# Optimization experiments

Hardware: AMD Instinct MI355X
Metric: run time of the kernel (lower is better)

The kernel has to match this reference:

```python
import jax, jax.numpy as jnp
import numpy as np

N = 8192  # nv + nh, bias=False


def setup_inputs() -> dict:
    key = jax.random.key(0)
    k1, k2, k3, k4 = jax.random.split(key, 4)
    w = jax.random.normal(k1, (N, N), dtype=jnp.float32) * 0.01  # learned [n,n] coupling matrix
    initial_state = jax.random.randint(k2, (N,), 0, 2).astype(jnp.float32)  # binary unit states
    clamping_degree = jnp.zeros((N,), dtype=jnp.float32)  # 0 => unit is free to update
    T = jnp.float32(1.0)  # temperature
    perm = jax.random.permutation(k3, N).astype(jnp.int32)  # torch.randperm(self.n)
    rand_u = jax.random.uniform(k4, (N,), dtype=jnp.float32)  # torch.rand(1) per unit
    return {"w": w, "initial_state": initial_state, "clamping_degree": clamping_degree,
            "T": T, "perm": perm, "rand_u": rand_u}


def reference(w, initial_state, clamping_degree, T, perm, rand_u):
    # Sequential Gibbs sweep: for each j in perm, if unclamped,
    # p = sigmoid(w[j]@state / T); state[j] = 1 if u <= p else 0.
    inactive = jnp.float32(0.0)

    def step(state, ju):
        j, u = ju
        sum_input = jnp.dot(w[j], state)          # per-unit dot product against current state
        p = jax.nn.sigmoid(sum_input / T)          # 1/(1+exp(-x/T))
        new_val = jnp.where(u <= p, jnp.float32(1.0), inactive)
        upd = jnp.where(clamping_degree[j] == 0, new_val, state[j])
        return state.at[j].set(upd), None

    final_state, _ = jax.lax.scan(step, initial_state, (perm, rand_u))
    return final_state
```

## Files before the change

kernel.cpp:

```cpp
#include <hip/hip_runtime.h>
#include <math.h>


#define NN 8192
#define BB 512
#define NBLK 16
#define SUB 64
#define NSUB 8
#define NWG 256
#define NWORK 255
#define TPB 512
#define MAXR 3

typedef unsigned int u32;

__global__ void k_init(u32* flags, int n) {
  int i = blockIdx.x * blockDim.x + threadIdx.x;
  for (; i < n; i += gridDim.x * blockDim.x) flags[i] = 0;
}

__device__ __forceinline__ u32 ld_rlx(const u32* p) {
  return __hip_atomic_load(p, __ATOMIC_RELAXED, __HIP_MEMORY_SCOPE_AGENT);
}
__device__ __forceinline__ void st_rlx(u32* p, u32 v) {
  __hip_atomic_store(p, v, __ATOMIC_RELAXED, __HIP_MEMORY_SCOPE_AGENT);
}
__device__ __forceinline__ float ldf_rlx(const float* p) {
  return __hip_atomic_load(p, __ATOMIC_RELAXED, __HIP_MEMORY_SCOPE_AGENT);
}
__device__ __forceinline__ void stf_rlx(float* p, float v) {
  __hip_atomic_store(p, v, __ATOMIC_RELAXED, __HIP_MEMORY_SCOPE_AGENT);
}
__device__ __forceinline__ double ldd_rlx(const double* p) {
  return __hip_atomic_load(p, __ATOMIC_RELAXED, __HIP_MEMORY_SCOPE_AGENT);
}
__device__ __forceinline__ void std_rlx(double* p, double v) {
  __hip_atomic_store(p, v, __ATOMIC_RELAXED, __HIP_MEMORY_SCOPE_AGENT);
}

#define LOADM(MARR, T8N) do {                                                  \
  const float4* mr_ = (const float4*)(tb + (size_t)((T8N) * SUB + tid) * BB + (T8N) * SUB); \
  _Pragma("unroll")                                                            \
  for (int j_ = 0; j_ < SUB / 4; ++j_) {                                       \
    float4 v_ = mr_[j_];                                                       \
    MARR[4*j_] = v_.x; MARR[4*j_+1] = v_.y;                                    \
    MARR[4*j_+2] = v_.z; MARR[4*j_+3] = v_.w; }                                \
} while (0)

#define CHAIN(MARR, T8C) do {                                                  \
  int row_ = (T8C) * SUB + tid;                                                \
  double sum_ = sumsL[row_], th_ = thrL[row_];                                 \
  float dd1_ = d1L[row_], dd0_ = d0L[row_];                                    \
  float mydel_ = 0.0f;                                                         \
  __builtin_amdgcn_s_setprio(3);                                               \
  _Pragma("unroll")                                                            \
  for (int s_ = 0; s_ < SUB; ++s_) {                                           \
    float down_ = (sum_ >= th_) ? dd1_ : dd0_;                                 \
    float sd_ = __uint_as_float(                                               \
        __builtin_amdgcn_readlane(__float_as_uint(down_), s_));                \
    if (s_ == tid) mydel_ = down_;                                             \
    sum_ += (double)(MARR[s_] * sd_); }                                        \
  __builtin_amdgcn_s_setprio(0);                                               \
  delL[row_] = mydel_;                                                         \
  if (pub) stf_rlx(&delG[b * BB + row_], mydel_);                              \
} while (0)

__global__ __launch_bounds__(TPB) void k_gibbs(
    const float* __restrict__ w, const float* __restrict__ init,
    const float* __restrict__ clampv, const float* __restrict__ Tp,
    const int* __restrict__ perm, const float* __restrict__ urand,
    float* __restrict__ dout, double* __restrict__ S,
    float* __restrict__ delG, float* __restrict__ tileD,
    u32* subFlag, u32* ack) {
  __shared__ float stateL[NN];
  __shared__ double sumsL[BB], thrL[BB];
  __shared__ float d1L[BB], d0L[BB], delL[BB], oldL[BB];
  __shared__ int uL[BB];
  __shared__ double redL[TPB / 64][MAXR];
  const int wg = blockIdx.x, tid = threadIdx.x;
  const int wv = tid >> 6, lane = tid & 63;

  if (wg == 0) {
    double T = (double)Tp[0];
    for (int b = 0; b < NBLK; ++b) {
      const bool pub = (b + 1 < NBLK);
      int pos = b * BB + tid;
      int unit = perm[pos];
      double uu = (double)urand[pos];
      thrL[tid] = T * log(uu / (1.0 - uu));
      float old = init[unit];
      bool cl = (clampv[unit] != 0.0f);
      d1L[tid] = cl ? 0.0f : (1.0f - old);
      d0L[tid] = cl ? 0.0f : (0.0f - old);
      oldL[tid] = old;
      uL[tid] = unit;
      {
        const u32* slots = ack + (size_t)b * NWORK;
        for (;;) {
          int ok = 1;
          if (tid < NWORK) ok = (ld_rlx(&slots[tid]) != 0u);
          if (__syncthreads_and(ok)) break;
          __builtin_amdgcn_s_sleep(1);
        }
      }
      sumsL[tid] = ldd_rlx(&S[(size_t)b * BB + tid]);
      __syncthreads();
      const float* tb = tileD + (size_t)b * BB * BB;
      float mA[SUB], mB[SUB];
      float4 nv0, nv1, nv2, nv3;
      if (tid < SUB) LOADM(mA, 0);

      for (int t8 = 0; t8 < NSUB; ++t8) {
        if (t8 > 0) {
          if (pub && tid == 0) st_rlx(&subFlag[b * NSUB + (t8 - 1)], 1u);
          if (tid >= 256) {
            int t = tid - 256;
            int rrow = t8 * SUB + (t >> 2);
            int q = t & 3;
            int c0 = (t8 - 1) * SUB + q * 16;
            double p_ =
                (double)(nv0.x * delL[c0])    + (double)(nv0.y * delL[c0+1]) +
                (double)(nv0.z * delL[c0+2])  + (double)(nv0.w * delL[c0+3]) +
                (double)(nv1.x * delL[c0+4])  + (double)(nv1.y * delL[c0+5]) +
                (double)(nv1.z * delL[c0+6])  + (double)(nv1.w * delL[c0+7]);
            p_ +=
                (double)(nv2.x * delL[c0+8])  + (double)(nv2.y * delL[c0+9]) +
                (double)(nv2.z * delL[c0+10]) + (double)(nv2.w * delL[c0+11]) +
                (double)(nv3.x * delL[c0+12]) + (double)(nv3.y * delL[c0+13]) +
                (double)(nv3.z * delL[c0+14]) + (double)(nv3.w * delL[c0+15]);
            p_ += __shfl_down(p_, 2, 4);
            p_ += __shfl_down(p_, 1, 4);
            if (q == 0) sumsL[rrow] += p_;
          }
        }
        __syncthreads();
        if (tid < SUB) {
          if (t8 & 1) { if (t8 < NSUB - 1) LOADM(mA, t8 + 1); CHAIN(mB, t8); }
          else        { if (t8 < NSUB - 1) LOADM(mB, t8 + 1); CHAIN(mA, t8); }
        } else {
          if (t8 < NSUB - 1 && tid >= 256) {
            int t = tid - 256;
            const float4* pr = (const float4*)(
                tb + (size_t)((t8 + 1) * SUB + (t >> 2)) * BB + t8 * SUB + (t & 3) * 16);
            nv0 = pr[0]; nv1 = pr[1]; nv2 = pr[2]; nv3 = pr[3];
          }
          if (t8 > 0) {
            for (int r = (t8 + 1) * SUB + (tid - SUB); r < BB; r += (TPB - SUB)) {
              int c0 = (t8 - 1) * SUB;
              const float4* mr3 = (const float4*)(tb + (size_t)r * BB + c0);
              double acc = sumsL[r];
#pragma unroll
              for (int j = 0; j < SUB / 4; ++j) {
                float4 v = mr3[j];
                acc += (double)(v.x * delL[c0+4*j])   + (double)(v.y * delL[c0+4*j+1]) +
                       (double)(v.z * delL[c0+4*j+2]) + (double)(v.w * delL[c0+4*j+3]);
              }
              sumsL[r] = acc;
            }
          }
        }
        __syncthreads();
      }
      if (pub && tid == 0) st_rlx(&subFlag[b * NSUB + (NSUB - 1)], 1u);
      dout[uL[tid]] = oldL[tid] + delL[tid];
    }
  } else {
    const int iw = wg - 1;
    const int r0 = (iw * BB) / NWORK, r1 = ((iw + 1) * BB) / NWORK;
    const int cnt = r1 - r0;
    for (int i = tid; i < NN; i += TPB) stateL[i] = init[i];
    __syncthreads();

    for (int p = 0; p < NBLK; ++p) {
      int pc = perm[p * BB + tid];
      float g[NSUB];
      float* tbp = tileD + (size_t)p * BB * BB;

      for (int ri = 0; ri < cnt; ++ri) {
        int unit = perm[p * BB + r0 + ri];
        const float* wrow = w + (size_t)unit * NN;
        const float4* wr4 = (const float4*)wrow;
        const float4* st4 = (const float4*)stateL;
        double acc = 0.0;
#pragma unroll
        for (int k = 0; k < NN / (4 * TPB); ++k) {
          float4 a = wr4[tid + k * TPB];
          float4 s = st4[tid + k * TPB];
          acc += (double)(a.x * s.x) + (double)(a.y * s.y) +
                 (double)(a.z * s.z) + (double)(a.w * s.w);
        }
        for (int o = 32; o > 0; o >>= 1) acc += __shfl_down(acc, o, 64);
        if (lane == 0) redL[wv][ri] = acc;
        stf_rlx(&tbp[(size_t)(r0 + ri) * BB + tid], wrow[pc]);
        if (p > 0 && wv == ri) {
#pragma unroll
          for (int t8 = 0; t8 < NSUB; ++t8)
            g[t8] = wrow[perm[(p - 1) * BB + t8 * SUB + lane]];
        }
      }
      __syncthreads();
      double Sr = 0.0;
      if (wv < cnt) {
#pragma unroll
        for (int k = 0; k < TPB / 64; ++k) Sr += redL[k][wv];
      }
      if (p > 0) {
        double crr = 0.0;
        for (int t8 = 0; t8 < NSUB; ++t8) {
          const u32* f = &subFlag[(p - 1) * NSUB + t8];
          if (tid == 0) {
            while (ld_rlx(f) == 0u) __builtin_amdgcn_s_sleep(1);
          }
          __syncthreads();
          float dl = ldf_rlx(&delG[(p - 1) * BB + t8 * SUB + lane]);
          if (wv < cnt) crr += (double)(g[t8] * dl);
          if (tid < SUB) stateL[perm[(p - 1) * BB + t8 * SUB + tid]] += dl;
        }
        for (int o = 32; o > 0; o >>= 1) crr += __shfl_down(crr, o, 64);
        Sr += crr;
      }
      if (wv < cnt && lane == 0) std_rlx(&S[(size_t)p * BB + r0 + wv], Sr);
      __syncthreads();
      if (tid == 0) st_rlx(&ack[(size_t)p * NWORK + iw], 1u);
    }
  }
}

extern "C" void kernel_launch(void* const* d_in, const int* in_sizes, int n_in,
                              void* d_out, int out_size, void* d_ws, size_t ws_size,
                              hipStream_t stream) {
  const float* w      = (const float*)d_in[0];
  const float* init   = (const float*)d_in[1];
  const float* clampv = (const float*)d_in[2];
  const float* Tp     = (const float*)d_in[3];
  const int*   perm   = (const int*)d_in[4];
  const float* urand  = (const float*)d_in[5];
  float* dout = (float*)d_out;

  double* S    = (double*)d_ws;
  float* delG  = (float*)(S + NN);
  float* tileD = delG + NN;
  u32* subFlag = (u32*)(tileD + (size_t)NBLK * BB * BB);
  u32* ack     = subFlag + NBLK * NSUB;

  int nflags = NBLK * NSUB + NBLK * NWORK;
  k_init<<<8, 256, 0, stream>>>(subFlag, nflags);

  void* args[] = {(void*)&w, (void*)&init, (void*)&clampv, (void*)&Tp,
                  (void*)&perm, (void*)&urand, (void*)&dout,
                  (void*)&S, (void*)&delG, (void*)&tileD,
                  (void*)&subFlag, (void*)&ack};
  hipLaunchCooperativeKernel((const void*)k_gibbs, dim3(NWG), dim3(TPB),
                             args, 0, stream);
}
```

Baseline: 508.6 us.

## Decouple worker blocks from last sub-block and stage diagonal tiles in LDS

```diff
diff --git a/kernel.cpp b/kernel.cpp
--- a/kernel.cpp
+++ b/kernel.cpp
@@ -11,8 +11,11 @@
 #define NWORK 255
 #define TPB 512
 #define MAXR 3
+#define MSTR 68
+#define MBUFW (SUB * MSTR)
 
 typedef unsigned int u32;
+typedef unsigned long long u64;
 
 __global__ void k_init(u32* flags, int n) {
   int i = blockIdx.x * blockDim.x + threadIdx.x;
@@ -37,115 +40,143 @@
 __device__ __forceinline__ void std_rlx(double* p, double v) {
   __hip_atomic_store(p, v, __ATOMIC_RELAXED, __HIP_MEMORY_SCOPE_AGENT);
 }
-
-#define LOADM(MARR, T8N) do {                                                  \
-  const float4* mr_ = (const float4*)(tb + (size_t)((T8N) * SUB + tid) * BB + (T8N) * SUB); \
-  _Pragma("unroll")                                                            \
-  for (int j_ = 0; j_ < SUB / 4; ++j_) {                                       \
-    float4 v_ = mr_[j_];                                                       \
-    MARR[4*j_] = v_.x; MARR[4*j_+1] = v_.y;                                    \
-    MARR[4*j_+2] = v_.z; MARR[4*j_+3] = v_.w; }                                \
-} while (0)
-
-#define CHAIN(MARR, T8C) do {                                                  \
-  int row_ = (T8C) * SUB + tid;                                                \
-  double sum_ = sumsL[row_], th_ = thrL[row_];                                 \
-  float dd1_ = d1L[row_], dd0_ = d0L[row_];                                    \
-  float mydel_ = 0.0f;                                                         \
-  __builtin_amdgcn_s_setprio(3);                                               \
-  _Pragma("unroll")                                                            \
-  for (int s_ = 0; s_ < SUB; ++s_) {                                           \
-    float down_ = (sum_ >= th_) ? dd1_ : dd0_;                                 \
-    float sd_ = __uint_as_float(                                               \
-        __builtin_amdgcn_readlane(__float_as_uint(down_), s_));                \
-    if (s_ == tid) mydel_ = down_;                                             \
-    sum_ += (double)(MARR[s_] * sd_); }                                        \
-  __builtin_amdgcn_s_setprio(0);                                               \
-  delL[row_] = mydel_;                                                         \
-  if (pub) stf_rlx(&delG[b * BB + row_], mydel_);                              \
-} while (0)
+__device__ __forceinline__ u64 ldq_rlx(const u64* p) {
+  return __hip_atomic_load(p, __ATOMIC_RELAXED, __HIP_MEMORY_SCOPE_AGENT);
+}
 
 __global__ __launch_bounds__(TPB) void k_gibbs(
     const float* __restrict__ w, const float* __restrict__ init,
     const float* __restrict__ clampv, const float* __restrict__ Tp,
     const int* __restrict__ perm, const float* __restrict__ urand,
-    float* __restrict__ dout, double* __restrict__ S,
-    float* __restrict__ delG, float* __restrict__ tileD,
+    float* __restrict__ dout,
+    double* __restrict__ thrG, double* __restrict__ S,
+    float* __restrict__ d1G, float* __restrict__ d0G,
+    float* __restrict__ oldG, float* __restrict__ delG,
+    float* __restrict__ stripG, float* __restrict__ tileD,
     u32* subFlag, u32* ack) {
-  __shared__ float stateL[NN];
-  __shared__ double sumsL[BB], thrL[BB];
-  __shared__ float d1L[BB], d0L[BB], delL[BB], oldL[BB];
-  __shared__ int uL[BB];
-  __shared__ double redL[TPB / 64][MAXR];
+  __shared__ double poolD[55296 / 8];
   const int wg = blockIdx.x, tid = threadIdx.x;
   const int wv = tid >> 6, lane = tid & 63;
 
   if (wg == 0) {
+    double* sumsL = poolD;
+    double* thrL  = poolD + BB;
+    float*  d1L   = (float*)(poolD + 2 * BB);
+    float*  d0L   = d1L + BB;
+    float*  delL  = d0L + BB;
+    float*  oldL  = delL + BB;
+    int*    uL    = (int*)(oldL + BB);
+    float*  mbuf  = (float*)(uL + BB);
+
     double T = (double)Tp[0];
+    for (int i = tid; i < NN; i += TPB) {
+      int unit = perm[i];
+      double uu = (double)urand[i];
+      std_rlx(&thrG[i], T * log(uu / (1.0 - uu)));
+      float old = init[unit];
+      bool cl = (clampv[unit] != 0.0f);
+      stf_rlx(&d1G[i], cl ? 0.0f : (1.0f - old));
+      stf_rlx(&d0G[i], cl ? 0.0f : (0.0f - old));
+      stf_rlx(&oldG[i], old);
+    }
+    __syncthreads();
+    {
+      const u32* slots = ack;
+      for (;;) {
+        int ok = 1;
+        if (tid < NWORK) ok = (ld_rlx(&slots[tid]) != 0u);
+        if (__syncthreads_and(ok)) break;
+        __builtin_amdgcn_s_sleep(1);
+      }
+    }
+    sumsL[tid] = ldd_rlx(&S[tid]);
+    thrL[tid] = ldd_rlx(&thrG[tid]);
+    d1L[tid] = ldf_rlx(&d1G[tid]);
+    d0L[tid] = ldf_rlx(&d0G[tid]);
+    oldL[tid] = ldf_rlx(&oldG[tid]);
+    uL[tid] = perm[tid];
+    if (tid >= 448) {
+      int l = tid - 448;
+      const float4* src = (const float4*)(tileD + (size_t)l * BB);
+      float4* dst = (float4*)(mbuf + l * MSTR);
+#pragma unroll
+      for (int j = 0; j < 16; ++j) dst[j] = src[j];
+    }
+    __syncthreads();
+
+    float4 nv0, nv1, nv2, nv3;
     for (int b = 0; b < NBLK; ++b) {
       const bool pub = (b + 1 < NBLK);
-      int pos = b * BB + tid;
-      int unit = perm[pos];
-      double uu = (double)urand[pos];
-      thrL[tid] = T * log(uu / (1.0 - uu));
-      float old = init[unit];
-      bool cl = (clampv[unit] != 0.0f);
-      d1L[tid] = cl ? 0.0f : (1.0f - old);
-      d0L[tid] = cl ? 0.0f : (0.0f - old);
-      oldL[tid] = old;
-      uL[tid] = unit;
-      {
-        const u32* slots = ack + (size_t)b * NWORK;
-        for (;;) {
-          int ok = 1;
-          if (tid < NWORK) ok = (ld_rlx(&slots[tid]) != 0u);
-          if (__syncthreads_and(ok)) break;
-          __builtin_amdgcn_s_sleep(1);
-        }
-      }
-      sumsL[tid] = ldd_rlx(&S[(size_t)b * BB + tid]);
-      __syncthreads();
       const float* tb = tileD + (size_t)b * BB * BB;
-      float mA[SUB], mB[SUB];
-      float4 nv0, nv1, nv2, nv3;
-      if (tid < SUB) LOADM(mA, 0);
 
       for (int t8 = 0; t8 < NSUB; ++t8) {
-        if (t8 > 0) {
-          if (pub && tid == 0) st_rlx(&subFlag[b * NSUB + (t8 - 1)], 1u);
-          if (tid >= 256) {
-            int t = tid - 256;
-            int rrow = t8 * SUB + (t >> 2);
-            int q = t & 3;
-            int c0 = (t8 - 1) * SUB + q * 16;
-            double p_ =
-                (double)(nv0.x * delL[c0])    + (double)(nv0.y * delL[c0+1]) +
-                (double)(nv0.z * delL[c0+2])  + (double)(nv0.w * delL[c0+3]) +
-                (double)(nv1.x * delL[c0+4])  + (double)(nv1.y * delL[c0+5]) +
-                (double)(nv1.z * delL[c0+6])  + (double)(nv1.w * delL[c0+7]);
-            p_ +=
-                (double)(nv2.x * delL[c0+8])  + (double)(nv2.y * delL[c0+9]) +
-                (double)(nv2.z * delL[c0+10]) + (double)(nv2.w * delL[c0+11]) +
-                (double)(nv3.x * delL[c0+12]) + (double)(nv3.y * delL[c0+13]) +
-                (double)(nv3.z * delL[c0+14]) + (double)(nv3.w * delL[c0+15]);
-            p_ += __shfl_down(p_, 2, 4);
-            p_ += __shfl_down(p_, 1, 4);
-            if (q == 0) sumsL[rrow] += p_;
-          }
-        }
-        __syncthreads();
+        int o = t8 * SUB;
+        float m[SUB];
+        if (t8 > 0 && pub && tid == 0) st_rlx(&subFlag[b * NSUB + t8 - 1], 1u);
         if (tid < SUB) {
-          if (t8 & 1) { if (t8 < NSUB - 1) LOADM(mA, t8 + 1); CHAIN(mB, t8); }
-          else        { if (t8 < NSUB - 1) LOADM(mB, t8 + 1); CHAIN(mA, t8); }
+          const float4* mr = (const float4*)(mbuf + (t8 & 1) * MBUFW + tid * MSTR);
+#pragma unroll
+          for (int j = 0; j < 16; ++j) {
+            float4 v = mr[j];
+            m[4*j] = v.x; m[4*j+1] = v.y; m[4*j+2] = v.z; m[4*j+3] = v.w;
+          }
+        } else if (t8 > 0 && tid >= 256) {
+          int t = tid - 256, g_ = t >> 2, q = t & 3;
+          int rrow = o + g_;
+          int c0 = (t8 - 1) * SUB + q * 16;
+          double p_ =
+              (double)(nv0.x * delL[c0])    + (double)(nv0.y * delL[c0+1]) +
+              (double)(nv0.z * delL[c0+2])  + (double)(nv0.w * delL[c0+3]) +
+              (double)(nv1.x * delL[c0+4])  + (double)(nv1.y * delL[c0+5]) +
+              (double)(nv1.z * delL[c0+6])  + (double)(nv1.w * delL[c0+7]);
+          p_ +=
+              (double)(nv2.x * delL[c0+8])  + (double)(nv2.y * delL[c0+9]) +
+              (double)(nv2.z * delL[c0+10]) + (double)(nv2.w * delL[c0+11]) +
+              (double)(nv3.x * delL[c0+12]) + (double)(nv3.y * delL[c0+13]) +
+              (double)(nv3.z * delL[c0+14]) + (double)(nv3.w * delL[c0+15]);
+          p_ += __shfl_down(p_, 2, 4);
+          p_ += __shfl_down(p_, 1, 4);
+          if (q == 0) sumsL[rrow] += p_;
+        }
+        __syncthreads();
+        if (tid < SUB) {
+          int row = o + tid;
+          double g = sumsL[row] - thrL[row];
+          float d1v = d1L[row], d0v = d0L[row];
+          u64 xb = 0ull;
+          __builtin_amdgcn_s_setprio(3);
+#pragma unroll
+          for (int s = 0; s < SUB; ++s) {
+            int hi = __builtin_amdgcn_readlane(
+                (int)(__double_as_longlong(g) >> 32), s);
+            int x = (hi >= 0) ? 1 : 0;
+            int a1 = __builtin_amdgcn_readlane((int)__float_as_uint(d1v), s);
+            int a0 = __builtin_amdgcn_readlane((int)__float_as_uint(d0v), s);
+            float sd = __uint_as_float((u32)(x ? a1 : a0));
+            g += (double)(m[s] * sd);
+            xb |= ((u64)x) << s;
+          }
+          __builtin_amdgcn_s_setprio(0);
+          float mydel = ((xb >> tid) & 1ull) ? d1v : d0v;
+          delL[row] = mydel;
+          if (pub) stf_rlx(&delG[b * BB + row], mydel);
+        } else if (tid < 128) {
+          if (t8 < NSUB - 1) {
+            int l = tid - 64, o2 = (t8 + 1) * SUB;
+            const float4* src = (const float4*)(tb + (size_t)(o2 + l) * BB + o2);
+            float4* dst = (float4*)(mbuf + ((t8 + 1) & 1) * MBUFW + l * MSTR);
+#pragma unroll
+            for (int j = 0; j < 16; ++j) dst[j] = src[j];
+          }
         } else {
           if (t8 < NSUB - 1 && tid >= 256) {
             int t = tid - 256;
             const float4* pr = (const float4*)(
-                tb + (size_t)((t8 + 1) * SUB + (t >> 2)) * BB + t8 * SUB + (t & 3) * 16);
+                tb + (size_t)((t8 + 1) * SUB + (t >> 2)) * BB + o + (t & 3) * 16);
             nv0 = pr[0]; nv1 = pr[1]; nv2 = pr[2]; nv3 = pr[3];
           }
           if (t8 > 0) {
-            for (int r = (t8 + 1) * SUB + (tid - SUB); r < BB; r += (TPB - SUB)) {
+            for (int r = (t8 + 1) * SUB + (tid - 128); r < BB; r += 384) {
               int c0 = (t8 - 1) * SUB;
               const float4* mr3 = (const float4*)(tb + (size_t)r * BB + c0);
               double acc = sumsL[r];
@@ -161,10 +192,53 @@
         }
         __syncthreads();
       }
-      if (pub && tid == 0) st_rlx(&subFlag[b * NSUB + (NSUB - 1)], 1u);
+      if (pub && tid == 0) st_rlx(&subFlag[b * NSUB + NSUB - 1], 1u);
       dout[uL[tid]] = oldL[tid] + delL[tid];
+      if (pub) {
+        {
+          const u32* slots = ack + (size_t)(b + 1) * NWORK;
+          for (;;) {
+            int ok = 1;
+            if (tid < NWORK) ok = (ld_rlx(&slots[tid]) != 0u);
+            if (__syncthreads_and(ok)) break;
+            __builtin_amdgcn_s_sleep(1);
+          }
+        }
+        {
+          double acc = ldd_rlx(&S[(size_t)(b + 1) * BB + tid]);
+          const u64* sp = (const u64*)(stripG + ((size_t)(b + 1) * BB + tid) * SUB);
+#pragma unroll
+          for (int k = 0; k < SUB / 2; ++k) {
+            u64 q = ldq_rlx(&sp[k]);
+            float f0 = __uint_as_float((u32)q);
+            float f1 = __uint_as_float((u32)(q >> 32));
+            acc += (double)(f0 * delL[448 + 2 * k]) +
+                   (double)(f1 * delL[448 + 2 * k + 1]);
+          }
+          sumsL[tid] = acc;
+        }
+        {
+          int pos = (b + 1) * BB + tid;
+          thrL[tid] = ldd_rlx(&thrG[pos]);
+          d1L[tid] = ldf_rlx(&d1G[pos]);
+          d0L[tid] = ldf_rlx(&d0G[pos]);
+          oldL[tid] = ldf_rlx(&oldG[pos]);
+          uL[tid] = perm[pos];
+        }
+        if (tid >= 448) {
+          int l = tid - 448;
+          const float4* src = (const float4*)(
+              tileD + (size_t)(b + 1) * BB * BB + (size_t)l * BB);
+          float4* dst = (float4*)(mbuf + l * MSTR);
+#pragma unroll
+          for (int j = 0; j < 16; ++j) dst[j] = src[j];
+        }
+        __syncthreads();
+      }
     }
   } else {
+    float* stateL = (float*)poolD;
+    double* redW = (double*)((char*)poolD + 32768);
     const int iw = wg - 1;
     const int r0 = (iw * BB) / NWORK, r1 = ((iw + 1) * BB) / NWORK;
     const int cnt = r1 - r0;
@@ -172,8 +246,17 @@
     __syncthreads();
 
     for (int p = 0; p < NBLK; ++p) {
+      if (p >= 2) {
+        const u32* f = &subFlag[(p - 2) * NSUB + NSUB - 1];
+        if (tid == 0) { while (ld_rlx(f) == 0u) __builtin_amdgcn_s_sleep(1); }
+        __syncthreads();
+        if (tid < SUB)
+          stateL[perm[(p - 2) * BB + 7 * SUB + tid]] +=
+              ldf_rlx(&delG[(p - 2) * BB + 7 * SUB + tid]);
+        __syncthreads();
+      }
       int pc = perm[p * BB + tid];
-      float g[NSUB];
+      float g[NSUB - 1];
       float* tbp = tileD + (size_t)p * BB * BB;
 
       for (int ri = 0; ri < cnt; ++ri) {
@@ -190,27 +273,28 @@
                  (double)(a.z * s.z) + (double)(a.w * s.w);
         }
         for (int o = 32; o > 0; o >>= 1) acc += __shfl_down(acc, o, 64);
-        if (lane == 0) redL[wv][ri] = acc;
+        if (lane == 0) redW[wv * MAXR + ri] = acc;
         stf_rlx(&tbp[(size_t)(r0 + ri) * BB + tid], wrow[pc]);
         if (p > 0 && wv == ri) {
 #pragma unroll
-          for (int t8 = 0; t8 < NSUB; ++t8)
+          for (int t8 = 0; t8 < NSUB - 1; ++t8)
             g[t8] = wrow[perm[(p - 1) * BB + t8 * SUB + lane]];
+          stf_rlx(&stripG[((size_t)p * BB + r0 + ri) * SUB + lane],
+                  wrow[perm[(p - 1) * BB + 7 * SUB + lane]]);
         }
       }
       __syncthreads();
       double Sr = 0.0;
       if (wv < cnt) {
 #pragma unroll
-        for (int k = 0; k < TPB / 64; ++k) Sr += redL[k][wv];
+        for (int k = 0; k < TPB / 64; ++k) Sr += redW[k * MAXR + wv];
       }
       if (p > 0) {
         double crr = 0.0;
-        for (int t8 = 0; t8 < NSUB; ++t8) {
+#pragma unroll
+        for (int t8 = 0; t8 < NSUB - 1; ++t8) {
           const u32* f = &subFlag[(p - 1) * NSUB + t8];
-          if (tid == 0) {
-            while (ld_rlx(f) == 0u) __builtin_amdgcn_s_sleep(1);
-          }
+          if (tid == 0) { while (ld_rlx(f) == 0u) __builtin_amdgcn_s_sleep(1); }
           __syncthreads();
           float dl = ldf_rlx(&delG[(p - 1) * BB + t8 * SUB + lane]);
           if (wv < cnt) crr += (double)(g[t8] * dl);
@@ -237,9 +321,14 @@
   const float* urand  = (const float*)d_in[5];
   float* dout = (float*)d_out;
 
-  double* S    = (double*)d_ws;
-  float* delG  = (float*)(S + NN);
-  float* tileD = delG + NN;
+  double* thrG = (double*)d_ws;
+  double* S    = thrG + NN;
+  float* d1G   = (float*)(S + NN);
+  float* d0G   = d1G + NN;
+  float* oldG  = d0G + NN;
+  float* delG  = oldG + NN;
+  float* stripG = delG + NN;
+  float* tileD = stripG + (size_t)NBLK * BB * SUB;
   u32* subFlag = (u32*)(tileD + (size_t)NBLK * BB * BB);
   u32* ack     = subFlag + NBLK * NSUB;
 
@@ -248,7 +337,8 @@
 
   void* args[] = {(void*)&w, (void*)&init, (void*)&clampv, (void*)&Tp,
                   (void*)&perm, (void*)&urand, (void*)&dout,
-                  (void*)&S, (void*)&delG, (void*)&tileD,
+                  (void*)&thrG, (void*)&S, (void*)&d1G, (void*)&d0G,
+                  (void*)&oldG, (void*)&delG, (void*)&stripG, (void*)&tileD,
                   (void*)&subFlag, (void*)&ack};
   hipLaunchCooperativeKernel((const void*)k_gibbs, dim3(NWG), dim3(TPB),
                              args, 0, stream);
```

Result: slower. 711.0 us (+39.8%).

## Restructure Gibbs chain with LDS-staged tiles, ballot-based sign test, and coarser sync

Applied to the files above, without the earlier changes.

```diff
diff --git a/kernel.cpp b/kernel.cpp
--- a/kernel.cpp
+++ b/kernel.cpp
@@ -11,8 +11,11 @@
 #define NWORK 255
 #define TPB 512
 #define MAXR 3
+#define MSTR 68
+#define MBUFW (SUB * MSTR)
 
 typedef unsigned int u32;
+typedef unsigned long long u64;
 
 __global__ void k_init(u32* flags, int n) {
   int i = blockIdx.x * blockDim.x + threadIdx.x;
@@ -37,33 +40,6 @@
 __device__ __forceinline__ void std_rlx(double* p, double v) {
   __hip_atomic_store(p, v, __ATOMIC_RELAXED, __HIP_MEMORY_SCOPE_AGENT);
 }
-
-#define LOADM(MARR, T8N) do {                                                  \
-  const float4* mr_ = (const float4*)(tb + (size_t)((T8N) * SUB + tid) * BB + (T8N) * SUB); \
-  _Pragma("unroll")                                                            \
-  for (int j_ = 0; j_ < SUB / 4; ++j_) {                                       \
-    float4 v_ = mr_[j_];                                                       \
-    MARR[4*j_] = v_.x; MARR[4*j_+1] = v_.y;                                    \
-    MARR[4*j_+2] = v_.z; MARR[4*j_+3] = v_.w; }                                \
-} while (0)
-
-#define CHAIN(MARR, T8C) do {                                                  \
-  int row_ = (T8C) * SUB + tid;                                                \
-  double sum_ = sumsL[row_], th_ = thrL[row_];                                 \
-  float dd1_ = d1L[row_], dd0_ = d0L[row_];                                    \
-  float mydel_ = 0.0f;                                                         \
-  __builtin_amdgcn_s_setprio(3);                                               \
-  _Pragma("unroll")                                                            \
-  for (int s_ = 0; s_ < SUB; ++s_) {                                           \
-    float down_ = (sum_ >= th_) ? dd1_ : dd0_;                                 \
-    float sd_ = __uint_as_float(                                               \
-        __builtin_amdgcn_readlane(__float_as_uint(down_), s_));                \
-    if (s_ == tid) mydel_ = down_;                                             \
-    sum_ += (double)(MARR[s_] * sd_); }                                        \
-  __builtin_amdgcn_s_setprio(0);                                               \
-  delL[row_] = mydel_;                                                         \
-  if (pub) stf_rlx(&delG[b * BB + row_], mydel_);                              \
-} while (0)
 
 __global__ __launch_bounds__(TPB) void k_gibbs(
     const float* __restrict__ w, const float* __restrict__ init,
@@ -71,16 +47,21 @@
     const int* __restrict__ perm, const float* __restrict__ urand,
     float* __restrict__ dout, double* __restrict__ S,
     float* __restrict__ delG, float* __restrict__ tileD,
-    u32* subFlag, u32* ack) {
-  __shared__ float stateL[NN];
-  __shared__ double sumsL[BB], thrL[BB];
-  __shared__ float d1L[BB], d0L[BB], delL[BB], oldL[BB];
-  __shared__ int uL[BB];
-  __shared__ double redL[TPB / 64][MAXR];
+    u32* delReady, u32* ack) {
+  __shared__ double poolD[55296 / 8];
   const int wg = blockIdx.x, tid = threadIdx.x;
   const int wv = tid >> 6, lane = tid & 63;
 
   if (wg == 0) {
+    double* sumsL = poolD;
+    double* thrL  = poolD + BB;
+    float*  d1L   = (float*)(poolD + 2 * BB);
+    float*  d0L   = d1L + BB;
+    float*  delL  = d0L + BB;
+    float*  oldL  = delL + BB;
+    int*    uL    = (int*)(oldL + BB);
+    float*  mbuf  = (float*)(uL + BB);
+
     double T = (double)Tp[0];
     for (int b = 0; b < NBLK; ++b) {
       const bool pub = (b + 1 < NBLK);
@@ -104,48 +85,82 @@
         }
       }
       sumsL[tid] = ldd_rlx(&S[(size_t)b * BB + tid]);
+      if (tid >= 448) {
+        int l = tid - 448;
+        const float4* src = (const float4*)(tileD + (size_t)b * BB * BB + (size_t)l * BB);
+        float4* dst = (float4*)(mbuf + l * MSTR);
+#pragma unroll
+        for (int j = 0; j < 16; ++j) dst[j] = src[j];
+      }
       __syncthreads();
       const float* tb = tileD + (size_t)b * BB * BB;
-      float mA[SUB], mB[SUB];
       float4 nv0, nv1, nv2, nv3;
-      if (tid < SUB) LOADM(mA, 0);
 
       for (int t8 = 0; t8 < NSUB; ++t8) {
-        if (t8 > 0) {
-          if (pub && tid == 0) st_rlx(&subFlag[b * NSUB + (t8 - 1)], 1u);
-          if (tid >= 256) {
-            int t = tid - 256;
-            int rrow = t8 * SUB + (t >> 2);
-            int q = t & 3;
-            int c0 = (t8 - 1) * SUB + q * 16;
-            double p_ =
-                (double)(nv0.x * delL[c0])    + (double)(nv0.y * delL[c0+1]) +
-                (double)(nv0.z * delL[c0+2])  + (double)(nv0.w * delL[c0+3]) +
-                (double)(nv1.x * delL[c0+4])  + (double)(nv1.y * delL[c0+5]) +
-                (double)(nv1.z * delL[c0+6])  + (double)(nv1.w * delL[c0+7]);
-            p_ +=
-                (double)(nv2.x * delL[c0+8])  + (double)(nv2.y * delL[c0+9]) +
-                (double)(nv2.z * delL[c0+10]) + (double)(nv2.w * delL[c0+11]) +
-                (double)(nv3.x * delL[c0+12]) + (double)(nv3.y * delL[c0+13]) +
-                (double)(nv3.z * delL[c0+14]) + (double)(nv3.w * delL[c0+15]);
-            p_ += __shfl_down(p_, 2, 4);
-            p_ += __shfl_down(p_, 1, 4);
-            if (q == 0) sumsL[rrow] += p_;
-          }
-        }
-        __syncthreads();
+        int o = t8 * SUB;
+        float m[SUB];
         if (tid < SUB) {
-          if (t8 & 1) { if (t8 < NSUB - 1) LOADM(mA, t8 + 1); CHAIN(mB, t8); }
-          else        { if (t8 < NSUB - 1) LOADM(mB, t8 + 1); CHAIN(mA, t8); }
+          const float4* mr = (const float4*)(mbuf + (t8 & 1) * MBUFW + tid * MSTR);
+#pragma unroll
+          for (int j = 0; j < 16; ++j) {
+            float4 v = mr[j];
+            m[4*j] = v.x; m[4*j+1] = v.y; m[4*j+2] = v.z; m[4*j+3] = v.w;
+          }
+        } else if (t8 > 0 && tid >= 256) {
+          int t = tid - 256, g_ = t >> 2, q = t & 3;
+          int rrow = o + g_;
+          int c0 = (t8 - 1) * SUB + q * 16;
+          double p_ =
+              (double)(nv0.x * delL[c0])    + (double)(nv0.y * delL[c0+1]) +
+              (double)(nv0.z * delL[c0+2])  + (double)(nv0.w * delL[c0+3]) +
+              (double)(nv1.x * delL[c0+4])  + (double)(nv1.y * delL[c0+5]) +
+              (double)(nv1.z * delL[c0+6])  + (double)(nv1.w * delL[c0+7]);
+          p_ +=
+              (double)(nv2.x * delL[c0+8])  + (double)(nv2.y * delL[c0+9]) +
+              (double)(nv2.z * delL[c0+10]) + (double)(nv2.w * delL[c0+11]) +
+              (double)(nv3.x * delL[c0+12]) + (double)(nv3.y * delL[c0+13]) +
+              (double)(nv3.z * delL[c0+14]) + (double)(nv3.w * delL[c0+15]);
+          p_ += __shfl_down(p_, 2, 4);
+          p_ += __shfl_down(p_, 1, 4);
+          if (q == 0) sumsL[rrow] += p_;
+        }
+        __syncthreads();
+        if (tid < SUB) {
+          float d1v = d1L[o + tid], d0v = d0L[o + tid];
+          u64 P1 = __ballot(d1v != 0.0f);
+          u64 M0 = __ballot(d0v != 0.0f);
+          double g = sumsL[o + tid] - thrL[o + tid];
+          u64 xb = 0ull;
+          __builtin_amdgcn_s_setprio(3);
+#pragma unroll
+          for (int s = 0; s < SUB; ++s) {
+            u32 t1 = ((P1 >> s) & 1ull) ? 0x3f800000u : 0u;
+            u32 t0 = ((M0 >> s) & 1ull) ? 0xbf800000u : 0u;
+            int hi = __builtin_amdgcn_readlane(
+                (int)(__double_as_longlong(g) >> 32), s);
+            float sdf = __uint_as_float((hi >= 0) ? t1 : t0);
+            g += (double)(m[s] * sdf);
+            xb |= ((u64)(hi >= 0 ? 1 : 0)) << s;
+          }
+          __builtin_amdgcn_s_setprio(0);
+          delL[o + tid] = ((xb >> tid) & 1ull) ? d1v : d0v;
+        } else if (tid < 128) {
+          if (t8 < NSUB - 1) {
+            int l = tid - 64, o2 = (t8 + 1) * SUB;
+            const float4* src = (const float4*)(tb + (size_t)(o2 + l) * BB + o2);
+            float4* dst = (float4*)(mbuf + ((t8 + 1) & 1) * MBUFW + l * MSTR);
+#pragma unroll
+            for (int j = 0; j < 16; ++j) dst[j] = src[j];
+          }
         } else {
           if (t8 < NSUB - 1 && tid >= 256) {
             int t = tid - 256;
             const float4* pr = (const float4*)(
-                tb + (size_t)((t8 + 1) * SUB + (t >> 2)) * BB + t8 * SUB + (t & 3) * 16);
+                tb + (size_t)((t8 + 1) * SUB + (t >> 2)) * BB + o + (t & 3) * 16);
             nv0 = pr[0]; nv1 = pr[1]; nv2 = pr[2]; nv3 = pr[3];
           }
           if (t8 > 0) {
-            for (int r = (t8 + 1) * SUB + (tid - SUB); r < BB; r += (TPB - SUB)) {
+            for (int r = (t8 + 1) * SUB + (tid - 128); r < BB; r += 384) {
               int c0 = (t8 - 1) * SUB;
               const float4* mr3 = (const float4*)(tb + (size_t)r * BB + c0);
               double acc = sumsL[r];
@@ -161,10 +176,16 @@
         }
         __syncthreads();
       }
-      if (pub && tid == 0) st_rlx(&subFlag[b * NSUB + (NSUB - 1)], 1u);
+      if (pub) {
+        stf_rlx(&delG[b * BB + tid], delL[tid]);
+        __syncthreads();
+        if (tid == 0) st_rlx(&delReady[b], 1u);
+      }
       dout[uL[tid]] = oldL[tid] + delL[tid];
     }
   } else {
+    float* stateL = (float*)poolD;
+    double* redW = (double*)((char*)poolD + 32768);
     const int iw = wg - 1;
     const int r0 = (iw * BB) / NWORK, r1 = ((iw + 1) * BB) / NWORK;
     const int cnt = r1 - r0;
@@ -190,7 +211,7 @@
                  (double)(a.z * s.z) + (double)(a.w * s.w);
         }
         for (int o = 32; o > 0; o >>= 1) acc += __shfl_down(acc, o, 64);
-        if (lane == 0) redL[wv][ri] = acc;
+        if (lane == 0) redW[wv * MAXR + ri] = acc;
         stf_rlx(&tbp[(size_t)(r0 + ri) * BB + tid], wrow[pc]);
         if (p > 0 && wv == ri) {
 #pragma unroll
@@ -202,26 +223,30 @@
       double Sr = 0.0;
       if (wv < cnt) {
 #pragma unroll
-        for (int k = 0; k < TPB / 64; ++k) Sr += redL[k][wv];
+        for (int k = 0; k < TPB / 64; ++k) Sr += redW[k * MAXR + wv];
       }
       if (p > 0) {
+        if (tid == 0) {
+          while (ld_rlx(&delReady[p - 1]) == 0u) __builtin_amdgcn_s_sleep(1);
+        }
+        __syncthreads();
         double crr = 0.0;
-        for (int t8 = 0; t8 < NSUB; ++t8) {
-          const u32* f = &subFlag[(p - 1) * NSUB + t8];
-          if (tid == 0) {
-            while (ld_rlx(f) == 0u) __builtin_amdgcn_s_sleep(1);
-          }
-          __syncthreads();
-          float dl = ldf_rlx(&delG[(p - 1) * BB + t8 * SUB + lane]);
-          if (wv < cnt) crr += (double)(g[t8] * dl);
-          if (tid < SUB) stateL[perm[(p - 1) * BB + t8 * SUB + tid]] += dl;
-        }
-        for (int o = 32; o > 0; o >>= 1) crr += __shfl_down(crr, o, 64);
-        Sr += crr;
+        if (wv < cnt) {
+#pragma unroll
+          for (int t8 = 0; t8 < NSUB; ++t8)
+            crr += (double)(g[t8] * ldf_rlx(&delG[(p - 1) * BB + t8 * SUB + lane]));
+          for (int o = 32; o > 0; o >>= 1) crr += __shfl_down(crr, o, 64);
+          Sr += crr;
+        }
       }
       if (wv < cnt && lane == 0) std_rlx(&S[(size_t)p * BB + r0 + wv], Sr);
       __syncthreads();
       if (tid == 0) st_rlx(&ack[(size_t)p * NWORK + iw], 1u);
+      if (p > 0) {
+        float dl = ldf_rlx(&delG[(p - 1) * BB + tid]);
+        stateL[perm[(p - 1) * BB + tid]] += dl;
+      }
+      __syncthreads();
     }
   }
 }
@@ -238,18 +263,18 @@
   float* dout = (float*)d_out;
 
   double* S    = (double*)d_ws;
-  float* delG  = (float*)(S + NN);
+  float* delG  = (float*)(S + (size_t)NBLK * BB);
   float* tileD = delG + NN;
-  u32* subFlag = (u32*)(tileD + (size_t)NBLK * BB * BB);
-  u32* ack     = subFlag + NBLK * NSUB;
-
-  int nflags = NBLK * NSUB + NBLK * NWORK;
-  k_init<<<8, 256, 0, stream>>>(subFlag, nflags);
+  u32* delReady = (u32*)(tileD + (size_t)NBLK * BB * BB);
+  u32* ack      = delReady + NBLK;
+
+  int nflags = NBLK + NBLK * NWORK;
+  k_init<<<8, 256, 0, stream>>>(delReady, nflags);
 
   void* args[] = {(void*)&w, (void*)&init, (void*)&clampv, (void*)&Tp,
                   (void*)&perm, (void*)&urand, (void*)&dout,
                   (void*)&S, (void*)&delG, (void*)&tileD,
-                  (void*)&subFlag, (void*)&ack};
+                  (void*)&delReady, (void*)&ack};
   hipLaunchCooperativeKernel((const void*)k_gibbs, dim3(NWG), dim3(TPB),
                              args, 0, stream);
 }
```

Result: slower. 589.4 us (+15.9%).

## Move last sub-block correction to sequential WG to shorten critical path

Applied to the files above, without the earlier changes.

```diff
diff --git a/kernel.cpp b/kernel.cpp
--- a/kernel.cpp
+++ b/kernel.cpp
@@ -13,6 +13,7 @@
 #define MAXR 3
 
 typedef unsigned int u32;
+typedef unsigned long long u64;
 
 __global__ void k_init(u32* flags, int n) {
   int i = blockIdx.x * blockDim.x + threadIdx.x;
@@ -30,9 +31,6 @@
 }
 __device__ __forceinline__ void stf_rlx(float* p, float v) {
   __hip_atomic_store(p, v, __ATOMIC_RELAXED, __HIP_MEMORY_SCOPE_AGENT);
-}
-__device__ __forceinline__ double ldd_rlx(const double* p) {
-  return __hip_atomic_load(p, __ATOMIC_RELAXED, __HIP_MEMORY_SCOPE_AGENT);
 }
 __device__ __forceinline__ void std_rlx(double* p, double v) {
   __hip_atomic_store(p, v, __ATOMIC_RELAXED, __HIP_MEMORY_SCOPE_AGENT);
@@ -70,8 +68,8 @@
     const float* __restrict__ clampv, const float* __restrict__ Tp,
     const int* __restrict__ perm, const float* __restrict__ urand,
     float* __restrict__ dout, double* __restrict__ S,
-    float* __restrict__ delG, float* __restrict__ tileD,
-    u32* subFlag, u32* ack) {
+    float* __restrict__ delG, float* __restrict__ stripG,
+    float* __restrict__ tileD, u32* subFlag, u32* ack) {
   __shared__ float stateL[NN];
   __shared__ double sumsL[BB], thrL[BB];
   __shared__ float d1L[BB], d0L[BB], delL[BB], oldL[BB];
@@ -103,7 +101,21 @@
           __builtin_amdgcn_s_sleep(1);
         }
       }
-      sumsL[tid] = ldd_rlx(&S[(size_t)b * BB + tid]);
+      {
+        double acc = S[(size_t)b * BB + tid];
+        if (b > 0) {
+          const float4* sp = (const float4*)(stripG + ((size_t)b * BB + tid) * SUB);
+#pragma unroll
+          for (int k = 0; k < SUB / 4; ++k) {
+            float4 v = sp[k];
+            acc += (double)(v.x * delL[7 * SUB + 4 * k]) +
+                   (double)(v.y * delL[7 * SUB + 4 * k + 1]) +
+                   (double)(v.z * delL[7 * SUB + 4 * k + 2]) +
+                   (double)(v.w * delL[7 * SUB + 4 * k + 3]);
+          }
+        }
+        sumsL[tid] = acc;
+      }
       __syncthreads();
       const float* tb = tileD + (size_t)b * BB * BB;
       float mA[SUB], mB[SUB];
@@ -172,8 +184,17 @@
     __syncthreads();
 
     for (int p = 0; p < NBLK; ++p) {
+      if (p >= 2) {
+        const u32* f = &subFlag[(p - 2) * NSUB + NSUB - 1];
+        if (tid == 0) { while (ld_rlx(f) == 0u) __builtin_amdgcn_s_sleep(1); }
+        __syncthreads();
+        if (tid < SUB)
+          stateL[perm[(p - 2) * BB + 7 * SUB + tid]] +=
+              ldf_rlx(&delG[(p - 2) * BB + 7 * SUB + tid]);
+        __syncthreads();
+      }
       int pc = perm[p * BB + tid];
-      float g[NSUB];
+      float g[NSUB - 1];
       float* tbp = tileD + (size_t)p * BB * BB;
 
       for (int ri = 0; ri < cnt; ++ri) {
@@ -194,8 +215,10 @@
         stf_rlx(&tbp[(size_t)(r0 + ri) * BB + tid], wrow[pc]);
         if (p > 0 && wv == ri) {
 #pragma unroll
-          for (int t8 = 0; t8 < NSUB; ++t8)
+          for (int t8 = 0; t8 < NSUB - 1; ++t8)
             g[t8] = wrow[perm[(p - 1) * BB + t8 * SUB + lane]];
+          stf_rlx(&stripG[((size_t)p * BB + r0 + ri) * SUB + lane],
+                  wrow[perm[(p - 1) * BB + 7 * SUB + lane]]);
         }
       }
       __syncthreads();
@@ -206,11 +229,10 @@
       }
       if (p > 0) {
         double crr = 0.0;
-        for (int t8 = 0; t8 < NSUB; ++t8) {
+#pragma unroll
+        for (int t8 = 0; t8 < NSUB - 1; ++t8) {
           const u32* f = &subFlag[(p - 1) * NSUB + t8];
-          if (tid == 0) {
-            while (ld_rlx(f) == 0u) __builtin_amdgcn_s_sleep(1);
-          }
+          if (tid == 0) { while (ld_rlx(f) == 0u) __builtin_amdgcn_s_sleep(1); }
           __syncthreads();
           float dl = ldf_rlx(&delG[(p - 1) * BB + t8 * SUB + lane]);
           if (wv < cnt) crr += (double)(g[t8] * dl);
@@ -238,8 +260,9 @@
   float* dout = (float*)d_out;
 
   double* S    = (double*)d_ws;
-  float* delG  = (float*)(S + NN);
-  float* tileD = delG + NN;
+  float* delG  = (float*)(S + (size_t)NBLK * BB);
+  float* stripG = delG + NN;
+  float* tileD = stripG + (size_t)NBLK * BB * SUB;
   u32* subFlag = (u32*)(tileD + (size_t)NBLK * BB * BB);
   u32* ack     = subFlag + NBLK * NSUB;
 
@@ -248,7 +271,7 @@
 
   void* args[] = {(void*)&w, (void*)&init, (void*)&clampv, (void*)&Tp,
                   (void*)&perm, (void*)&urand, (void*)&dout,
-                  (void*)&S, (void*)&delG, (void*)&tileD,
+                  (void*)&S, (void*)&delG, (void*)&stripG, (void*)&tileD,
                   (void*)&subFlag, (void*)&ack};
   hipLaunchCooperativeKernel((const void*)k_gibbs, dim3(NWG), dim3(TPB),
                              args, 0, stream);
```

Measured after the change: 566.9 us. +11.4%, slower.
